# Kernel tuning notes

Measured on AMD Instinct MI355X. Metric: run time of the kernel, lower is better.

Reference implementation:

```python
import jax, jax.numpy as jnp
import numpy as np
from jax import lax

DIM = 256; RESO = 64; STRIPE = 8; NH = 8
HSP, WSP = RESO, STRIPE   # attention_mode=0: vertical stripes
HD = DIM // NH
B = 8; L = RESO * RESO
WIN = HSP * WSP           # tokens per window (512)


def _vertical_mask():
    # Faithful to verticalAttnMask: column labels 0/1/2 over last stripe, then
    # window-partition and pairwise-compare.
    shift = STRIPE // 2
    lab = np.zeros(RESO, np.float32)
    lab[RESO - STRIPE:RESO - shift] = 1.0
    lab[RESO - shift:] = 2.0
    img = np.broadcast_to(lab[None, :], (RESO, RESO))            # [H, W]
    # shiftedWindowVerticalPartition with reso=RESO, stripes=STRIPE
    mw = img.reshape(RESO, RESO // STRIPE, STRIPE).transpose(1, 0, 2).reshape(-1, WIN)
    diff = mw[:, None, :] - mw[:, :, None]                        # [nW, L, L]
    return jnp.asarray(np.where(diff != 0.0, -100.0, 0.0).astype(np.float32))

_MASK = _vertical_mask()  # [nW=8, 512, 512]


def _seq2cswin(x):
    Bx = x.shape[0]
    img = x.transpose(0, 2, 1).reshape(Bx, DIM, RESO, RESO)
    w = img.reshape(Bx, DIM, RESO // HSP, HSP, RESO // WSP, WSP)
    w = w.transpose(0, 2, 4, 3, 5, 1).reshape(-1, WIN, DIM)
    return w.reshape(-1, WIN, NH, HD).transpose(0, 2, 1, 3)


def _forward(qkv, scale, proj_w, proj_b, conv_w, conv_b):
    q, k, v = qkv[0], qkv[1], qkv[2]
    qw = _seq2cswin(q) * scale[0]
    kw = _seq2cswin(k)
    # get_lepe: window-partition v as images, depthwise 3x3 conv
    vimg = v.transpose(0, 2, 1).reshape(B, DIM, RESO, RESO)
    vwin = vimg.reshape(B, DIM, RESO // HSP, HSP, RESO // WSP, WSP)
    vwin = vwin.transpose(0, 2, 4, 1, 3, 5).reshape(-1, DIM, HSP, WSP)  # [B*nW, C, Hsp, Wsp]
    lepe = lax.conv_general_dilated(
        vwin, conv_w, (1, 1), ((1, 1), (1, 1)),
        dimension_numbers=('NCHW', 'OIHW', 'NCHW'), feature_group_count=DIM
    ) + conv_b[None, :, None, None]
    lepe = lepe.reshape(-1, NH, HD, WIN).transpose(0, 1, 3, 2)
    vw = vwin.reshape(-1, NH, HD, WIN).transpose(0, 1, 3, 2)
    attn = jnp.einsum('wnid,wnjd->wnij', qw, kw)
    # currentDepth odd, mode 0 -> vertical shifted-window mask
    attn = attn + jnp.tile(_MASK, (B, 1, 1))[:, None, :, :]
    attn = jax.nn.softmax(attn, axis=-1)
    x = jnp.einsum('wnij,wnjd->wnid', attn, vw) + lepe
    x = x.transpose(0, 2, 1, 3).reshape(-1, WIN, DIM)
    x = x @ proj_w.T + proj_b
    # CSwin2img then flatten back to [B, L, C]
    x = x.reshape(B, RESO // HSP, RESO // WSP, HSP, WSP, DIM)
    x = x.transpose(0, 1, 3, 2, 4, 5).reshape(B, RESO, RESO, DIM)
    return x.reshape(B, L, DIM)


def setup_inputs() -> dict:
    key = jax.random.key(0)
    ks = jax.random.split(key, 5)
    qkv = jax.random.normal(ks[0], (3, B, L, DIM), jnp.float32)
    scale = jnp.full((1,), HD ** (-0.5), jnp.float32)
    proj_w = jax.random.normal(ks[1], (DIM, DIM), jnp.float32) * (DIM ** -0.5)
    proj_b = jax.random.normal(ks[2], (DIM,), jnp.float32) * 0.02
    conv_w = jax.random.normal(ks[3], (DIM, 1, 3, 3), jnp.float32) * 0.1
    conv_b = jax.random.normal(ks[4], (DIM,), jnp.float32) * 0.02
    return {"qkv": qkv, "scale": scale, "proj_w": proj_w, "proj_b": proj_b,
            "conv_w": conv_w, "conv_b": conv_b}


def reference(qkv, scale, proj_w, proj_b, conv_w, conv_b):
    return _forward(qkv, scale, proj_w, proj_b, conv_w, conv_b)
```

## Files before the change

### kernel.cpp

```cpp
#include <hip/hip_runtime.h>
#include <hip/hip_bf16.h>

#define BATCH 8
#define NH    8
#define HD    32
#define WIN   512
#define DIM   256
#define RESO  64
#define SEQL  4096
#define VSTRIDE 520
#define WPAD  264

#define LOG2E 1.44269504088896340736f

extern "C" __device__ float __ocml_native_exp2_f32(float);

typedef __attribute__((ext_vector_type(8))) short short8;
typedef __attribute__((ext_vector_type(4))) float floatx4;

__device__ __forceinline__ unsigned short f2bf(float f) {
    union { float f; unsigned int i; } x; x.f = f;
    unsigned int r = x.i + 0x7fff + ((x.i >> 16) & 1);
    return (unsigned short)(r >> 16);
}
__device__ __forceinline__ float bf2f(unsigned short u) {
    union { unsigned int i; float f; } x; x.i = ((unsigned int)u) << 16; return x.f;
}
__device__ __forceinline__ unsigned int pk2(float lo, float hi) {
    return ((unsigned int)f2bf(hi) << 16) | (unsigned int)f2bf(lo);
}
__device__ __forceinline__ unsigned int pk2t(float lo, float hi) {
    union { float f; unsigned int i; } a, b; a.f = lo; b.f = hi;
    return __builtin_amdgcn_perm(b.i, a.i, 0x07060302);
}
__device__ __forceinline__ void unp2(unsigned int u, float& lo, float& hi) {
    union { unsigned int i; float f; } a, b;
    a.i = u << 16; b.i = u & 0xffff0000u;
    lo = a.f; hi = b.f;
}

union FragU {
    unsigned int  u[4];
    unsigned short us[8];
    short8        s;
    ushort4       v4[2];
};

__global__ __launch_bounds__(512, 4)
void attn_mfma_kernel(const float* __restrict__ qkv,
                      const float* __restrict__ scale_p,
                      const float* __restrict__ conv_w,
                      const float* __restrict__ conv_b,
                      unsigned short* __restrict__ X)
{
    __shared__ alignas(16) unsigned short Klds[WIN * HD];
    __shared__ alignas(16) unsigned short Vt[HD * VSTRIDE];
    __shared__ float cw[HD * 9];
    __shared__ float cb[HD];

    const int wh   = blockIdx.x;
    const int bw   = wh >> 3;
    const int head = wh & 7;
    const int b    = bw >> 3;
    const int wx   = bw & 7;
    const int tid  = threadIdx.x;

    const float scale = scale_p[0] * LOG2E;
    const size_t plane = (size_t)BATCH * SEQL * DIM;
    const float* qg = qkv;
    const float* kg = qkv + plane;
    const float* vg = qkv + 2 * plane;

    for (int idx = tid; idx < WIN * 4; idx += 512) {
        const int t = idx >> 2, c8 = idx & 3;
        const size_t goff = ((size_t)b * SEQL + (size_t)(t >> 3) * RESO + wx * 8 + (t & 7)) * DIM
                          + head * HD + c8 * 8;
        const float4 k0 = *(const float4*)(kg + goff);
        const float4 k1 = *(const float4*)(kg + goff + 4);
        uint4 pk;
        pk.x = pk2t(k0.x, k0.y); pk.y = pk2t(k0.z, k0.w);
        pk.z = pk2t(k1.x, k1.y); pk.w = pk2t(k1.z, k1.w);
        const int p = c8 ^ ((t >> 1) & 3);
        *(uint4*)&Klds[t * HD + p * 8] = pk;
    }
    for (int idx = tid; idx < 256 * HD; idx += 512) {
        const int ch = idx & 31, tp = idx >> 5;
        const int t = tp * 2;
        const size_t goff = ((size_t)b * SEQL + (size_t)(t >> 3) * RESO + wx * 8 + (t & 7)) * DIM
                          + head * HD + ch;
        const float v0 = vg[goff];
        const float v1 = vg[goff + DIM];
        *(unsigned int*)&Vt[ch * VSTRIDE + t] = pk2(v0, v1);
    }
    for (int i = tid; i < HD * 9; i += 512) cw[i] = conv_w[head * HD * 9 + i];
    if (tid < HD) cb[tid] = conv_b[head * HD + tid];
    __syncthreads();

    const int lane = tid & 63, wid = tid >> 6;
    const int q4 = lane >> 4, nn = lane & 15;
    const int qbase = wid * 64;
    const bool mwin = (wx == 7);

    float mk[4];
    #pragma unroll
    for (int r = 0; r < 4; ++r) {
        const bool kgrp = (((q4 * 4 + r) & 7) < 4);
        const bool qgrp = ((nn & 7) < 4);
        mk[r] = (kgrp != qgrp) ? (-100.f * LOG2E) : 0.f;
    }

    short8 qf[4];
    #pragma unroll
    for (int qq = 0; qq < 4; ++qq) {
        const int t = qbase + qq * 16 + nn;
        const size_t goff = ((size_t)b * SEQL + (size_t)(t >> 3) * RESO + wx * 8 + (t & 7)) * DIM
                          + head * HD + q4 * 8;
        const float4 a = *(const float4*)(qg + goff);
        const float4 c = *(const float4*)(qg + goff + 4);
        FragU f;
        f.u[0] = pk2t(a.x * scale, a.y * scale);
        f.u[1] = pk2t(a.z * scale, a.w * scale);
        f.u[2] = pk2t(c.x * scale, c.y * scale);
        f.u[3] = pk2t(c.z * scale, c.w * scale);
        qf[qq] = f.s;
    }

    floatx4 acc[4][2];
    #pragma unroll
    for (int qq = 0; qq < 4; ++qq) {
        acc[qq][0] = (floatx4){0.f, 0.f, 0.f, 0.f};
        acc[qq][1] = (floatx4){0.f, 0.f, 0.f, 0.f};
    }
    float rs[4] = {0.f, 0.f, 0.f, 0.f};
    const floatx4 zf = (floatx4){0.f, 0.f, 0.f, 0.f};

    for (int kc = 0; kc < 16; ++kc) {
        short8 kf0, kf1;
        {
            const int t0 = (2 * kc) * 16 + nn;
            const int t1 = (2 * kc + 1) * 16 + nn;
            kf0 = *(const short8*)&Klds[t0 * HD + (q4 ^ ((t0 >> 1) & 3)) * 8];
            kf1 = *(const short8*)&Klds[t1 * HD + (q4 ^ ((t1 >> 1) & 3)) * 8];
        }
        short8 vf[2];
        #pragma unroll
        for (int nt = 0; nt < 2; ++nt) {
            const int ch = nt * 16 + nn;
            FragU f;
            f.v4[0] = *(const ushort4*)&Vt[ch * VSTRIDE + kc * 32 + q4 * 4];
            f.v4[1] = *(const ushort4*)&Vt[ch * VSTRIDE + kc * 32 + 16 + q4 * 4];
            vf[nt] = f.s;
        }
        #pragma unroll
        for (int qq = 0; qq < 4; ++qq) {
            floatx4 s0 = __builtin_amdgcn_mfma_f32_16x16x32_bf16(kf0, qf[qq], zf, 0, 0, 0);
            floatx4 s1 = __builtin_amdgcn_mfma_f32_16x16x32_bf16(kf1, qf[qq], zf, 0, 0, 0);
            if (mwin) {
                #pragma unroll
                for (int r = 0; r < 4; ++r) { s0[r] += mk[r]; s1[r] += mk[r]; }
            }
            float p[8];
            #pragma unroll
            for (int r = 0; r < 4; ++r) {
                p[r]     = __ocml_native_exp2_f32(s0[r]);
                p[4 + r] = __ocml_native_exp2_f32(s1[r]);
            }
            rs[qq] += ((p[0] + p[1]) + (p[2] + p[3])) + ((p[4] + p[5]) + (p[6] + p[7]));
            FragU pf;
            pf.u[0] = pk2t(p[0], p[1]);
            pf.u[1] = pk2t(p[2], p[3]);
            pf.u[2] = pk2t(p[4], p[5]);
            pf.u[3] = pk2t(p[6], p[7]);
            acc[qq][0] = __builtin_amdgcn_mfma_f32_16x16x32_bf16(vf[0], pf.s, acc[qq][0], 0, 0, 0);
            acc[qq][1] = __builtin_amdgcn_mfma_f32_16x16x32_bf16(vf[1], pf.s, acc[qq][1], 0, 0, 0);
        }
    }

    float inv[4];
    #pragma unroll
    for (int qq = 0; qq < 4; ++qq) {
        float v = rs[qq];
        v += __shfl_xor(v, 16);
        v += __shfl_xor(v, 32);
        inv[qq] = 1.0f / v;
    }

    #pragma unroll
    for (int qq = 0; qq < 4; ++qq) {
        const int t = qbase + qq * 16 + nn;
        const int h = t >> 3, wi = t & 7;
        #pragma unroll
        for (int nt = 0; nt < 2; ++nt) {
            const int chb = nt * 16 + q4 * 4;
            float o[4];
            #pragma unroll
            for (int r = 0; r < 4; ++r)
                o[r] = acc[qq][nt][r] * inv[qq] + cb[chb + r];
            #pragma unroll
            for (int dh = -1; dh <= 1; ++dh) {
                const int hh = h + dh;
                if (hh < 0 || hh >= RESO) continue;
                #pragma unroll
                for (int dw = -1; dw <= 1; ++dw) {
                    const int ww = wi + dw;
                    if (ww < 0 || ww >= 8) continue;
                    const int tj  = hh * 8 + ww;
                    const int wof = (dh + 1) * 3 + (dw + 1);
                    #pragma unroll
                    for (int r = 0; r < 4; ++r)
                        o[r] += cw[(chb + r) * 9 + wof] * bf2f(Vt[(chb + r) * VSTRIDE + tj]);
                }
            }
            ushort4 st;
            st.x = f2bf(o[0]); st.y = f2bf(o[1]); st.z = f2bf(o[2]); st.w = f2bf(o[3]);
            *(ushort4*)&X[((size_t)bw * WIN + t) * DIM + head * HD + chb] = st;
        }
    }
}

__global__ __launch_bounds__(256, 4)
void proj_mfma_kernel(const unsigned short* __restrict__ X,
                      const float* __restrict__ pw,
                      const float* __restrict__ pb,
                      float* __restrict__ out)
{
    __shared__ alignas(16) unsigned short Wl[64 * WPAD];

    const int bx   = blockIdx.x;
    const int mblk = bx >> 2;
    const int nblk = bx & 3;
    const int tid  = threadIdx.x;
    const int n0   = nblk * 64;

    {
        const int row = tid >> 2;
        const int cb0 = (tid & 3) * 64;
        #pragma unroll
        for (int c = 0; c < 64; c += 8) {
            const float4 w0 = *(const float4*)&pw[(size_t)(n0 + row) * DIM + cb0 + c];
            const float4 w1 = *(const float4*)&pw[(size_t)(n0 + row) * DIM + cb0 + c + 4];
            uint4 pk;
            pk.x = pk2(w0.x, w0.y); pk.y = pk2(w0.z, w0.w);
            pk.z = pk2(w1.x, w1.y); pk.w = pk2(w1.z, w1.w);
            *(uint4*)&Wl[row * WPAD + cb0 + c] = pk;
        }
    }
    __syncthreads();

    const int lane = tid & 63, wid = tid >> 6;
    const int q4 = lane >> 4, nn = lane & 15;
    const int mwave = mblk * 256 + wid * 64;

    floatx4 acc[4][4];
    #pragma unroll
    for (int i = 0; i < 4; ++i)
        #pragma unroll
        for (int j = 0; j < 4; ++j)
            acc[i][j] = (floatx4){0.f, 0.f, 0.f, 0.f};

    for (int kk = 0; kk < 8; ++kk) {
        short8 af[4], bf[4];
        #pragma unroll
        for (int nt = 0; nt < 4; ++nt)
            af[nt] = *(const short8*)&Wl[(nt * 16 + nn) * WPAD + kk * 32 + q4 * 8];
        #pragma unroll
        for (int mt = 0; mt < 4; ++mt) {
            const int m = mwave + mt * 16 + nn;
            bf[mt] = *(const short8*)&X[(size_t)m * DIM + kk * 32 + q4 * 8];
        }
        #pragma unroll
        for (int nt = 0; nt < 4; ++nt)
            #pragma unroll
            for (int mt = 0; mt < 4; ++mt)
                acc[nt][mt] = __builtin_amdgcn_mfma_f32_16x16x32_bf16(af[nt], bf[mt], acc[nt][mt], 0, 0, 0);
    }

    float4 bias[4];
    #pragma unroll
    for (int nt = 0; nt < 4; ++nt)
        bias[nt] = *(const float4*)&pb[n0 + nt * 16 + q4 * 4];

    size_t rowoff[4];
    #pragma unroll
    for (int mt = 0; mt < 4; ++mt) {
        const int m  = mwave + mt * 16 + nn;
        const int bw = m >> 9, t = m & 511;
        const int bb = bw >> 3, wx = bw & 7, hh = t >> 3, wi = t & 7;
        rowoff[mt] = ((size_t)bb * SEQL + (size_t)hh * RESO + wx * 8 + wi) * DIM;
    }

    #pragma unroll
    for (int nt = 0; nt < 4; ++nt)
        #pragma unroll
        for (int mt = 0; mt < 4; ++mt) {
            float4 v;
            v.x = acc[nt][mt][0] + bias[nt].x;
            v.y = acc[nt][mt][1] + bias[nt].y;
            v.z = acc[nt][mt][2] + bias[nt].z;
            v.w = acc[nt][mt][3] + bias[nt].w;
            *(float4*)&out[rowoff[mt] + n0 + nt * 16 + q4 * 4] = v;
        }
}

extern "C" void kernel_launch(void* const* d_in, const int* in_sizes, int n_in,
                              void* d_out, int out_size, void* d_ws, size_t ws_size,
                              hipStream_t stream)
{
    const float* qkv    = (const float*)d_in[0];
    const float* scale  = (const float*)d_in[1];
    const float* proj_w = (const float*)d_in[2];
    const float* proj_b = (const float*)d_in[3];
    const float* conv_w = (const float*)d_in[4];
    const float* conv_b = (const float*)d_in[5];

    unsigned short* X = (unsigned short*)d_ws;

    attn_mfma_kernel<<<dim3(BATCH * NH * 8), dim3(512), 0, stream>>>(
        qkv, scale, conv_w, conv_b, X);

    proj_mfma_kernel<<<dim3(512), dim3(256), 0, stream>>>(
        X, proj_w, proj_b, (float*)d_out);
}
```

Before: 215.1 us.

## Prefetch K/V fragments, remap block order, and overlap Q loads with staging

Both the attention and projection kernels now remap blockIdx so that consecutive blocks are spread across XCD-sized groups, aiming for better L2 locality. In the attention kernel, the K/V staging loops are fully unrolled, the Q fragment loads are moved ahead of the barrier, and the inner loop software-pipelines the next chunk's K/V LDS fragments while the current MFMAs run. s_setprio is raised around the MFMA section. The prefetch adds register pressure at 4 blocks/SM, and the wrap-around prefetch on the final iteration reads redundant data.

New measurement: 213.4 us. No clear change (-0.8%).

```diff
diff --git a/kernel.cpp b/kernel.cpp
--- a/kernel.cpp
+++ b/kernel.cpp
@@ -32,11 +32,6 @@
 __device__ __forceinline__ unsigned int pk2t(float lo, float hi) {
     union { float f; unsigned int i; } a, b; a.f = lo; b.f = hi;
     return __builtin_amdgcn_perm(b.i, a.i, 0x07060302);
-}
-__device__ __forceinline__ void unp2(unsigned int u, float& lo, float& hi) {
-    union { unsigned int i; float f; } a, b;
-    a.i = u << 16; b.i = u & 0xffff0000u;
-    lo = a.f; hi = b.f;
 }
 
 union FragU {
@@ -58,7 +53,8 @@
     __shared__ float cw[HD * 9];
     __shared__ float cb[HD];
 
-    const int wh   = blockIdx.x;
+    const int wh_raw = blockIdx.x;
+    const int wh   = ((wh_raw & 7) << 6) | (wh_raw >> 3);
     const int bw   = wh >> 3;
     const int head = wh & 7;
     const int b    = bw >> 3;
@@ -71,7 +67,9 @@
     const float* kg = qkv + plane;
     const float* vg = qkv + 2 * plane;
 
-    for (int idx = tid; idx < WIN * 4; idx += 512) {
+    #pragma unroll
+    for (int kk = 0; kk < 4; ++kk) {
+        const int idx = tid + kk * 512;
         const int t = idx >> 2, c8 = idx & 3;
         const size_t goff = ((size_t)b * SEQL + (size_t)(t >> 3) * RESO + wx * 8 + (t & 7)) * DIM
                           + head * HD + c8 * 8;
@@ -83,7 +81,9 @@
         const int p = c8 ^ ((t >> 1) & 3);
         *(uint4*)&Klds[t * HD + p * 8] = pk;
     }
-    for (int idx = tid; idx < 256 * HD; idx += 512) {
+    #pragma unroll
+    for (int kk = 0; kk < 16; ++kk) {
+        const int idx = tid + kk * 512;
         const int ch = idx & 31, tp = idx >> 5;
         const int t = tp * 2;
         const size_t goff = ((size_t)b * SEQL + (size_t)(t >> 3) * RESO + wx * 8 + (t & 7)) * DIM
@@ -92,22 +92,13 @@
         const float v1 = vg[goff + DIM];
         *(unsigned int*)&Vt[ch * VSTRIDE + t] = pk2(v0, v1);
     }
-    for (int i = tid; i < HD * 9; i += 512) cw[i] = conv_w[head * HD * 9 + i];
-    if (tid < HD) cb[tid] = conv_b[head * HD + tid];
-    __syncthreads();
+    if (tid < HD * 9) cw[tid] = conv_w[head * HD * 9 + tid];
+    if (tid < HD)     cb[tid] = conv_b[head * HD + tid];
 
     const int lane = tid & 63, wid = tid >> 6;
     const int q4 = lane >> 4, nn = lane & 15;
     const int qbase = wid * 64;
     const bool mwin = (wx == 7);
-
-    float mk[4];
-    #pragma unroll
-    for (int r = 0; r < 4; ++r) {
-        const bool kgrp = (((q4 * 4 + r) & 7) < 4);
-        const bool qgrp = ((nn & 7) < 4);
-        mk[r] = (kgrp != qgrp) ? (-100.f * LOG2E) : 0.f;
-    }
 
     short8 qf[4];
     #pragma unroll
@@ -124,6 +115,15 @@
         f.u[3] = pk2t(c.z * scale, c.w * scale);
         qf[qq] = f.s;
     }
+    __syncthreads();
+
+    float mk[4];
+    #pragma unroll
+    for (int r = 0; r < 4; ++r) {
+        const bool kgrp = (((q4 * 4 + r) & 7) < 4);
+        const bool qgrp = ((nn & 7) < 4);
+        mk[r] = (kgrp != qgrp) ? (-100.f * LOG2E) : 0.f;
+    }
 
     floatx4 acc[4][2];
     #pragma unroll
@@ -134,23 +134,39 @@
     float rs[4] = {0.f, 0.f, 0.f, 0.f};
     const floatx4 zf = (floatx4){0.f, 0.f, 0.f, 0.f};
 
+    const int kswz = (q4 ^ ((nn >> 1) & 3)) * 8;
+    const unsigned short* kp0 = &Klds[nn * HD + kswz];
+    const unsigned short* kp1 = &Klds[(16 + nn) * HD + kswz];
+    const unsigned short* vp0 = &Vt[nn * VSTRIDE + q4 * 4];
+    const unsigned short* vp1 = &Vt[(16 + nn) * VSTRIDE + q4 * 4];
+
+    short8 kf0 = *(const short8*)kp0;
+    short8 kf1 = *(const short8*)kp1;
+    short8 vf0, vf1;
+    {
+        FragU f0, f1;
+        f0.v4[0] = *(const ushort4*)vp0;
+        f0.v4[1] = *(const ushort4*)(vp0 + 16);
+        f1.v4[0] = *(const ushort4*)vp1;
+        f1.v4[1] = *(const ushort4*)(vp1 + 16);
+        vf0 = f0.s; vf1 = f1.s;
+    }
+
     for (int kc = 0; kc < 16; ++kc) {
-        short8 kf0, kf1;
+        const int nko = ((kc + 1) & 15) * 32;
+        short8 nkf0 = *(const short8*)(kp0 + nko * HD);
+        short8 nkf1 = *(const short8*)(kp1 + nko * HD);
+        short8 nvf0, nvf1;
         {
-            const int t0 = (2 * kc) * 16 + nn;
-            const int t1 = (2 * kc + 1) * 16 + nn;
-            kf0 = *(const short8*)&Klds[t0 * HD + (q4 ^ ((t0 >> 1) & 3)) * 8];
-            kf1 = *(const short8*)&Klds[t1 * HD + (q4 ^ ((t1 >> 1) & 3)) * 8];
-        }
-        short8 vf[2];
-        #pragma unroll
-        for (int nt = 0; nt < 2; ++nt) {
-            const int ch = nt * 16 + nn;
-            FragU f;
-            f.v4[0] = *(const ushort4*)&Vt[ch * VSTRIDE + kc * 32 + q4 * 4];
-            f.v4[1] = *(const ushort4*)&Vt[ch * VSTRIDE + kc * 32 + 16 + q4 * 4];
-            vf[nt] = f.s;
-        }
+            FragU f0, f1;
+            f0.v4[0] = *(const ushort4*)(vp0 + nko);
+            f0.v4[1] = *(const ushort4*)(vp0 + nko + 16);
+            f1.v4[0] = *(const ushort4*)(vp1 + nko);
+            f1.v4[1] = *(const ushort4*)(vp1 + nko + 16);
+            nvf0 = f0.s; nvf1 = f1.s;
+        }
+
+        __builtin_amdgcn_s_setprio(1);
         #pragma unroll
         for (int qq = 0; qq < 4; ++qq) {
             floatx4 s0 = __builtin_amdgcn_mfma_f32_16x16x32_bf16(kf0, qf[qq], zf, 0, 0, 0);
@@ -171,9 +187,12 @@
             pf.u[1] = pk2t(p[2], p[3]);
             pf.u[2] = pk2t(p[4], p[5]);
             pf.u[3] = pk2t(p[6], p[7]);
-            acc[qq][0] = __builtin_amdgcn_mfma_f32_16x16x32_bf16(vf[0], pf.s, acc[qq][0], 0, 0, 0);
-            acc[qq][1] = __builtin_amdgcn_mfma_f32_16x16x32_bf16(vf[1], pf.s, acc[qq][1], 0, 0, 0);
-        }
+            acc[qq][0] = __builtin_amdgcn_mfma_f32_16x16x32_bf16(vf0, pf.s, acc[qq][0], 0, 0, 0);
+            acc[qq][1] = __builtin_amdgcn_mfma_f32_16x16x32_bf16(vf1, pf.s, acc[qq][1], 0, 0, 0);
+        }
+        __builtin_amdgcn_s_setprio(0);
+
+        kf0 = nkf0; kf1 = nkf1; vf0 = nvf0; vf1 = nvf1;
     }
 
     float inv[4];
@@ -226,7 +245,8 @@
 {
     __shared__ alignas(16) unsigned short Wl[64 * WPAD];
 
-    const int bx   = blockIdx.x;
+    const int bx_raw = blockIdx.x;
+    const int bx   = ((bx_raw & 7) << 6) | (bx_raw >> 3);
     const int mblk = bx >> 2;
     const int nblk = bx & 3;
     const int tid  = threadIdx.x;
```
